# Optimization experiments

Measured on AMD Instinct MI355X. Metric: run time of the kernel, lower is better.

Reference implementation:

```python
import jax, jax.numpy as jnp
import numpy as np

# ---- static hyperparameters (mirror init_kwargs) ----
L_MAX = 3
N_MAX_L = [8, 6, 4, 2]            # radial basis size per l (precomputer.n_max_l)
N_CHANNELS = 32                   # num_element_channels
K_MAX_L = [n * N_CHANNELS for n in N_MAX_L]   # [256, 192, 128, 64]
SH_SIZES = [2 * l + 1 for l in range(L_MAX + 1)]  # [1,3,5,7]
MP_SCALING = 0.1
NU_SCALING = 0.1
NU_MAX = 2                        # max_correlation_order_per_layer
N_LAYERS = 2                      # num_message_passing_layers

# Fixed CG coupling tensors for all valid (l1, l2, L) with |l1-l2|<=L<=min(l1+l2, L_MAX).
# (Deterministic stand-ins for real Clebsch-Gordan coefficients; same sparsity/coupling
# structure and identical in fwd and fwdbwd modules.)
_rng = np.random.RandomState(0)
CG = {}
for _l1 in range(L_MAX + 1):
    for _l2 in range(L_MAX + 1):
        for _L in range(abs(_l1 - _l2), min(_l1 + _l2, L_MAX) + 1):
            CG[(_l1, _l2, _L)] = jnp.asarray(
                (_rng.randn(2 * _l1 + 1, 2 * _l2 + 1, 2 * _L + 1) * 0.2).astype(np.float32))


def split_l(x, sizes):
    out, i = [], 0
    for s in sizes:
        out.append(x[:, i:i + s])
        i += s
    return out


def embed_centers(feats, emb):
    # feats[l]: [N, 2l+1, n_l*C]; multiply channel block c by per-atom embedding emb[:, c]
    C = emb.shape[1]
    out = []
    for f in feats:
        n, m, k = f.shape
        out.append((f.reshape(n, m, k // C, C) * emb[:, None, None, :]).reshape(n, m, k))
    return out


def tensor_product(A, B):
    # per-atom CG tensor product, channel-aligned with truncation to min k
    n = A[0].shape[0]
    out = [jnp.zeros((n, 2 * L + 1, K_MAX_L[L]), A[0].dtype) for L in range(L_MAX + 1)]
    for (l1, l2, L), cg in CG.items():
        kk = min(K_MAX_L[l1], K_MAX_L[l2], K_MAX_L[L])
        t = jnp.einsum('nak,nbk,abM->nMk', A[l1][:, :, :kk], B[l2][:, :, :kk], cg)
        out[L] = out[L].at[:, :, :kk].add(t)
    return out


def cg_iterate(feats):
    # CGIterator: nu_max-1 iterated tensor products with residual accumulation
    g = feats
    for _ in range(NU_MAX - 1):
        tp = tensor_product(g, feats)
        g = [g[l] + NU_SCALING * tp[l] for l in range(L_MAX + 1)]
    return g


def invariant_mp(rb_l, sh_l, centers, emb_nbr, n_atoms):
    # spherical expansion: scatter rb x sh x neighbor-embedding over pairs -> centers
    out = []
    for l in range(L_MAX + 1):
        # [P, 2l+1, n_l, C] -> [P, 2l+1, k_l]
        msg = sh_l[l][:, :, None, None] * rb_l[l][:, None, :, None] * emb_nbr[:, None, None, :]
        msg = msg.reshape(msg.shape[0], 2 * l + 1, -1)
        out.append(MP_SCALING * jax.ops.segment_sum(msg, centers, num_segments=n_atoms))
    return out


def equivariant_mp(rb_l, sh_l, centers, neighbors, feats, n_atoms):
    # pair messages: CG-couple radially weighted SH edge features with neighbor features
    edge = [sh_l[l] * rb_l[l].sum(-1, keepdims=True) for l in range(L_MAX + 1)]  # [P, 2l+1]
    out = [jnp.zeros((n_atoms, 2 * L + 1, K_MAX_L[L]), feats[0].dtype) for L in range(L_MAX + 1)]
    for (l1, l2, L), cg in CG.items():
        kk = min(K_MAX_L[l2], K_MAX_L[L])
        w = jnp.einsum('pa,abM->pbM', edge[l1], cg)        # [P, 2l2+1, 2L+1]
        fg = feats[l2][neighbors, :, :kk]                   # gather: [P, 2l2+1, kk]
        msg = jnp.einsum('pbM,pbk->pMk', w, fg)             # [P, 2L+1, kk]
        out[L] = out[L].at[:, :, :kk].add(
            MP_SCALING * jax.ops.segment_sum(msg, centers, num_segments=n_atoms))
    return out


def setup_inputs() -> dict:
    key = jax.random.key(0)
    ks = jax.random.split(key, 8)
    N, P = 5000, 100000
    return {
        'sh': jax.random.normal(ks[0], (P, sum(SH_SIZES)), dtype=jnp.float32),
        'rb': jax.random.uniform(ks[1], (P, sum(N_MAX_L)), dtype=jnp.float32),
        'emb_table': jax.random.normal(ks[2], (4, N_CHANNELS), dtype=jnp.float32),
        'w_energy': jax.random.normal(ks[3], (K_MAX_L[0], 1), dtype=jnp.float32) * 0.05,
        'b_energy': jax.random.normal(ks[4], (1,), dtype=jnp.float32),
        'species_idx': jax.random.randint(ks[5], (N,), 0, 4, dtype=jnp.int32),
        'centers': jax.random.randint(ks[6], (P,), 0, N, dtype=jnp.int32),
        'neighbors': jax.random.randint(ks[7], (P,), 0, N, dtype=jnp.int32),
    }


def reference(sh, rb, emb_table, w_energy, b_energy, species_idx, centers, neighbors):
    n_atoms = species_idx.shape[0]
    sh_l = split_l(sh * NU_SCALING, SH_SIZES)   # nu_scaling applied to spherical harmonics
    rb_l = split_l(rb, N_MAX_L)
    center_emb = emb_table[species_idx]          # [N, C]
    emb_nbr = center_emb[neighbors]              # [P, C]
    # invariant message passing -> spherical expansion, then first CG iteration
    feats = invariant_mp(rb_l, sh_l, centers, emb_nbr, n_atoms)
    feats = cg_iterate(feats)
    # remaining equivariant message-passing layers
    for _ in range(N_LAYERS - 1):
        ef = embed_centers(feats, center_emb)
        mp = equivariant_mp(rb_l, sh_l, centers, neighbors, ef, n_atoms)
        feats = cg_iterate(mp)
    feats = embed_centers(feats, center_emb)
    energies = feats[0] @ w_energy + b_energy    # [N, 1, 1]
    return energies
```

## Files before the change

kernel.cpp:

```cpp
#include <hip/hip_runtime.h>
#include <vector>
#include <cmath>
#include <cstdint>

constexpr int KLc[4]  = {256,192,128,64};
constexpr int NMLc[4] = {8,6,4,2};
constexpr int SHBc[5] = {0,1,4,9,16};
constexpr int RBBc[5] = {0,8,14,18,20};
constexpr int FBc[5]  = {0,256,832,1472,1920};
constexpr int NCMB = 34, CGTOT = 3436, FTOT = 1920;

struct Combos { int l1[NCMB], l2[NCMB], L[NCMB], cgoff[NCMB], kk[NCMB]; };
constexpr Combos make_combos(){
  Combos c{}; int n=0, cg=0;
  for(int a=0;a<=3;a++)for(int b=0;b<=3;b++){
    int lo=a>b?a-b:b-a, hi=(a+b<3)?(a+b):3;
    for(int L=lo;L<=hi;L++){
      c.l1[n]=a; c.l2[n]=b; c.L[n]=L; c.cgoff[n]=cg;
      int mx=a>b?a:b; if(L>mx) mx=L; c.kk[n]=KLc[mx];
      cg+=(2*a+1)*(2*b+1)*(2*L+1); n++;
    }
  }
  return c;
}
constexpr Combos CB = make_combos();
static_assert(CB.cgoff[NCMB-1] + 7*7*7 == CGTOT, "cg size");

struct Grp { int cnt[4]; int list[4][12]; };
constexpr Grp make_Lg(){ Grp g{}; for(int i=0;i<NCMB;i++){ int L=CB.L[i]; g.list[L][g.cnt[L]++]=i; } return g; }
constexpr Grp LG = make_Lg();

struct Rows { int sh[64], rb[64], off[64]; };
constexpr Rows make_rows(){ Rows r{}; int i=0;
  for(int l=0;l<4;l++)for(int m=0;m<2*l+1;m++)for(int n=0;n<NMLc[l];n++){
    r.sh[i]=SHBc[l]+m; r.rb[i]=RBBc[l]+n; r.off[i]=FBc[l]+m*KLc[l]+n*32; i++; }
  for(;i<64;i++){ r.sh[i]=0; r.rb[i]=0; r.off[i]=0; }
  return r; }
constexpr Rows RWS = make_rows();

constexpr int NSL=425, NG=8, MAXS=56, MAXR=12, RPAD=149;

constexpr int iabs_(int x){ return x<0?-x:x; }
__host__ __device__ constexpr bool sl_valid(int l1,int l2,int kt){ return l2<=3-kt && iabs_(l1-l2)<=3-kt; }

__host__ __device__ constexpr int rb_base(int kt,int l1,int l2){
  int base=0;
  for(int p=0;p<4;p++)for(int q=0;q<4;q++){
    if(p==l1 && q==l2) return base;
    if(sl_valid(p,q,kt)) base += (2*p+1)*(2*q+1);
  }
  return base;
}

struct EqTab {
  int ns[NG];
  unsigned char eidx[NG][MAXS];
  unsigned char fidx[NG][MAXS];
  short         srow[NG][MAXS];
  unsigned char sph [NG][MAXS];
  int nr[NG];
  short roff[NG][MAXR];
  int total;
};
constexpr EqTab make_eqtab(){
  EqTab T{}; int gidx=0;
  for(int l2=0;l2<4;l2++)for(int kt=0;kt<4-l2;kt++)for(int b=0;b<2*l2+1;b++){
    const int rowoff = FBc[l2] + b*KLc[l2] + kt*64;
    for(int l1=0;l1<4;l1++){
      if(!sl_valid(l1,l2,kt)) continue;
      for(int a=0;a<2*l1+1;a++){
        int g = (gidx*NG)/NSL;
        int s = T.ns[g]++;
        T.eidx[g][s] = (unsigned char)(SHBc[l1]+a);
        int rbi = rb_base(kt,l1,l2) + a*(2*l2+1) + b;
        int ph, sr;
        if(kt==0){ if(l1<=2){ ph=0; sr=rbi; } else { ph=1; sr=rbi-144; } }
        else { ph=kt+1; sr=rbi; }
        T.sph[g][s]=(unsigned char)ph; T.srow[g][s]=(short)sr;
        int ri=-1;
        for(int r=0;r<T.nr[g];r++) if(T.roff[g][r]==(short)rowoff) ri=r;
        if(ri<0){ ri=T.nr[g]; T.roff[g][T.nr[g]++]=(short)rowoff; }
        T.fidx[g][s]=(unsigned char)ri;
        gidx++;
      }
    }
  }
  T.total=gidx;
  return T;
}
constexpr EqTab ET = make_eqtab();
static_assert(ET.total==NSL, "slice count");
constexpr bool chk_ns(){ for(int g=0;g<NG;g++) if(ET.ns[g]>MAXS) return false; return true; }
constexpr bool chk_nr(){ for(int g=0;g<NG;g++) if(ET.nr[g]>MAXR) return false; return true; }
static_assert(chk_ns(), "MAXS");
static_assert(chk_nr(), "MAXR");

struct CAsg { int cnt[NG]; unsigned char ci[NG][8]; };
constexpr CAsg make_casg(){
  CAsg C{}; bool used[NCMB]{}; int load[NG]{};
  for(int it=0; it<NCMB; it++){
    int best=-1, bc=-1;
    for(int i=0;i<NCMB;i++) if(!used[i]){
      int c=(2*CB.l1[i]+1)*(2*CB.l2[i]+1)*(2*CB.L[i]+1);
      if(c>bc){bc=c;best=i;}
    }
    used[best]=true;
    int g=0; for(int j=1;j<NG;j++) if(load[j]<load[g]) g=j;
    C.ci[g][C.cnt[g]++]=(unsigned char)best; load[g]+=bc;
  }
  return C;
}
constexpr CAsg CA = make_casg();
constexpr bool chk_ca(){ for(int g=0;g<NG;g++) if(CA.cnt[g]>8) return false; return true; }
static_assert(chk_ca(), "CA cap");

__host__ __device__ constexpr bool combo_in_phase(int ci,int ph){
  int l1=CB.l1[ci], l2=CB.l2[ci], L=CB.L[ci];
  if(ph==0) return l1<=2;
  if(ph==1) return l1==3;
  int kt=ph-1;
  return (l2<=3-kt) && (L<=3-kt);
}
__host__ __device__ constexpr int phase_kt(int ph){ return ph<=1?0:ph-1; }
__host__ __device__ constexpr int phase_rbadj(int ph){ return ph==1?144:0; }

namespace nprng {
struct MT {
  uint32_t mt[624]; int mti; bool has_g; double g;
  void seed(uint32_t s){ for(int i=0;i<624;i++){ mt[i]=s; s=1812433253u*(s^(s>>30))+(uint32_t)i+1u; } mti=624; has_g=false; g=0.0; }
  uint32_t u32(){
    if(mti>=624){
      for(int i=0;i<624;i++){
        uint32_t y=(mt[i]&0x80000000u)|(mt[(i+1)%624]&0x7fffffffu);
        mt[i]=mt[(i+397)%624]^(y>>1)^((y&1u)?0x9908b0dfu:0u);
      }
      mti=0;
    }
    uint32_t y=mt[mti++];
    y^=y>>11; y^=(y<<7)&0x9d2c5680u; y^=(y<<15)&0xefc60000u; y^=y>>18;
    return y;
  }
  double dbl(){ uint32_t a=u32()>>5, b=u32()>>6; return (a*67108864.0+b)/9007199254740992.0; }
  double gauss(){
    if(has_g){ has_g=false; return g; }
    double f,x1,x2,r2;
    do{ x1=2.0*dbl()-1.0; x2=2.0*dbl()-1.0; r2=x1*x1+x2*x2; }while(r2>=1.0||r2==0.0);
    f=sqrt(-2.0*log(r2)/r2);
    g=f*x1; has_g=true; return f*x2;
  }
};
}
static std::vector<float> build_cg(){
  nprng::MT r; r.seed(0);
  std::vector<float> v; v.reserve(CGTOT);
  for(int l1=0;l1<=3;l1++)for(int l2=0;l2<=3;l2++){
    int lo = l1>l2? l1-l2 : l2-l1;
    int hi = (l1+l2<3)? (l1+l2) : 3;
    for(int L=lo;L<=hi;L++){
      int n=(2*l1+1)*(2*l2+1)*(2*L+1);
      for(int i=0;i<n;i++) v.push_back((float)(r.gauss()*0.2));
    }
  }
  return v;
}

__global__ __launch_bounds__(256) void k_cemb(const float* __restrict__ emb_table,
    const int* __restrict__ species, float* __restrict__ cemb, int* __restrict__ counts, int N){
  int i = blockIdx.x*256 + threadIdx.x;
  if(i < N) counts[i] = 0;
  if(i < N*32){ int n = i>>5, c = i&31; cemb[i] = emb_table[species[n]*32 + c]; }
}

__global__ __launch_bounds__(256) void k_hist(const int* __restrict__ centers, int* counts, int P){
  int i = blockIdx.x*256 + threadIdx.x;
  if(i < P) atomicAdd(&counts[centers[i]], 1);
}

__global__ __launch_bounds__(256) void k_scan(const int* __restrict__ counts,
    int* __restrict__ offsets, int* __restrict__ cursor, int N){
  __shared__ int part[256];
  const int t = threadIdx.x;
  const int CH = (N + 255)/256;
  const int lo = t*CH;
  int hi = (t+1)*CH; if(hi > N) hi = N;
  int s = 0;
  for(int i=lo;i<hi;i++) s += counts[i];
  part[t] = s; __syncthreads();
  const int own = s;
  for(int d=1; d<256; d<<=1){
    int v = (t>=d)? part[t-d] : 0;
    __syncthreads();
    part[t] += v;
    __syncthreads();
  }
  int run = part[t] - own;
  for(int i=lo;i<hi;i++){ offsets[i]=run; cursor[i]=run; run += counts[i]; }
  if(t==255) offsets[N] = part[255];
}

__global__ __launch_bounds__(256) void k_scatter(const int* __restrict__ centers,
    int* cursor, int* __restrict__ perm, int P){
  int i = blockIdx.x*256 + threadIdx.x;
  if(i < P){ int c = centers[i]; int pos = atomicAdd(&cursor[c], 1); perm[pos] = i; }
}

__global__ __launch_bounds__(256) void k_inv(const float* __restrict__ sh, const float* __restrict__ rb,
    const float* __restrict__ cemb, const int* __restrict__ nbrs, const int* __restrict__ offsets,
    const int* __restrict__ perm, float* __restrict__ feats){
  const int a = blockIdx.x, t = threadIdx.x;
  __shared__ float sh_s[8][16], rb_s[8][20], emb_s[8][32], shrb_s[8][60];
  const int c = t & 31, rg = t >> 5;
  float acc[8];
  #pragma unroll
  for(int j=0;j<8;j++) acc[j] = 0.f;
  const int beg = offsets[a], cnt = offsets[a+1]-beg;
  for(int jb=0; jb<cnt; jb+=8){
    __syncthreads();
    for(int u=t; u<8*36; u+=256){
      int j=u/36, i=u-36*j;
      if(jb+j<cnt){
        int p=perm[beg+jb+j];
        if(i<16) sh_s[j][i]=sh[p*16+i]*0.1f;
        else     rb_s[j][i-16]=rb[p*20+i-16];
      }
    }
    for(int u=t; u<8*32; u+=256){
      int j=u>>5, i=u&31;
      if(jb+j<cnt){ int nb=nbrs[perm[beg+jb+j]]; emb_s[j][i]=cemb[(size_t)nb*32+i]; }
    }
    __syncthreads();
    for(int u=t; u<8*60; u+=256){
      int j=u/60, r=u-60*j;
      if(jb+j<cnt) shrb_s[j][r] = sh_s[j][RWS.sh[r]] * rb_s[j][RWS.rb[r]];
    }
    __syncthreads();
    const int jm = (cnt-jb<8)?(cnt-jb):8;
    for(int j=0;j<jm;j++){
      const float e = emb_s[j][c];
      #pragma unroll
      for(int q=0;q<8;q++){ int r=rg+8*q; if(r<60) acc[q]=fmaf(shrb_s[j][r], e, acc[q]); }
    }
  }
  #pragma unroll
  for(int q=0;q<8;q++){
    int r = rg + 8*q;
    if(r < 60) feats[(size_t)a*FTOT + RWS.off[r] + c] = 0.1f * acc[q];
  }
}

__device__ __forceinline__ float cg_u(const float* __restrict__ cg, int idx){
  return cg[__builtin_amdgcn_readfirstlane(idx)];
}
__global__ __launch_bounds__(256) void k_tp(float* __restrict__ feats, const float* __restrict__ cg){
  const int a = blockIdx.x, t = threadIdx.x;
  __shared__ float f_s[FTOT];
  float* fa = feats + (size_t)a*FTOT;
  for(int i=t;i<FTOT;i+=256)  f_s[i]  = fa[i];
  __syncthreads();
  #pragma unroll
  for(int L=0; L<4; L++){
    const int KLL = KLc[L], nL = 2*L+1;
    const int nel = nL*KLL;
    for(int e=t; e<nel; e+=256){
      const int M = e / KLL, k = e - M*KLL;
      float acc = 0.f;
      #pragma unroll
      for(int gi=0; gi<LG.cnt[L]; gi++){
        const int ci = LG.list[L][gi];
        const int l1 = CB.l1[ci], l2 = CB.l2[ci];
        if(k < CB.kk[ci]){
          const int n2 = 2*l2+1;
          #pragma unroll
          for(int aa=0; aa<2*l1+1; aa++){
            const float Av = f_s[FBc[l1] + aa*KLc[l1] + k];
            #pragma unroll
            for(int b=0; b<n2; b++)
              acc += cg_u(cg, CB.cgoff[ci] + (aa*n2+b)*nL + M) * (Av * f_s[FBc[l2] + b*KLc[l2] + k]);
          }
        }
      }
      fa[FBc[L] + M*KLL + k] = f_s[FBc[L] + M*KLL + k] + 0.1f*acc;
    }
  }
}

template<int G,int PH,int U>
__device__ __forceinline__ void contract_combos(const float* __restrict__ stageT,
    float* __restrict__ out_s, const float* __restrict__ cg, int lane){
  if constexpr (U < CA.cnt[G]) {
    constexpr int ci = CA.ci[G][U];
    if constexpr (combo_in_phase(ci,PH)) {
      constexpr int l1=CB.l1[ci], l2=CB.l2[ci], L=CB.L[ci];
      constexpr int n1=2*l1+1, n2=2*l2+1, nL=2*L+1;
      constexpr int kt=phase_kt(PH);
      constexpr int rbase = rb_base(kt,l1,l2) - phase_rbadj(PH);
      float oa[nL];
      #pragma unroll
      for(int M=0;M<nL;M++) oa[M]=0.f;
      #pragma unroll
      for(int aa=0;aa<n1;aa++){
        #pragma unroll
        for(int b=0;b<n2;b++){
          const float sv = stageT[lane*RPAD + rbase + aa*n2 + b];
          #pragma unroll
          for(int M=0;M<nL;M++)
            oa[M] = fmaf(cg[CB.cgoff[ci] + (aa*n2+b)*nL + M], sv, oa[M]);
        }
      }
      #pragma unroll
      for(int M=0;M<nL;M++)
        atomicAdd(&out_s[FBc[L] + M*KLc[L] + kt*64 + lane], oa[M]);
    }
    contract_combos<G,PH,U+1>(stageT,out_s,cg,lane);
  }
}

template<int G,int PH>
__device__ __forceinline__ void eq_phase(const float* acc, float* stageT, float* out_s,
    const float* __restrict__ cg, int lane){
  __syncthreads();
  #pragma unroll
  for(int s=0;s<ET.ns[G];s++){
    if(ET.sph[G][s]==PH) stageT[lane*RPAD + ET.srow[G][s]] = acc[s];
  }
  __syncthreads();
  contract_combos<G,PH,0>(stageT,out_s,cg,lane);
}

template<int G>
__device__ __forceinline__ void eq_group_main(
    const int a, const int t, const int lane,
    const float* __restrict__ sh, const float* __restrict__ rb,
    const float* __restrict__ cemb, const int* __restrict__ nbrs,
    const int* __restrict__ offsets, const int* __restrict__ perm,
    const float* __restrict__ featsA, float* __restrict__ featsB,
    const float* __restrict__ cg,
    float* stageT, float* out_s, float* edge_s, int* nb_s){
  constexpr int NS = ET.ns[G], NR = ET.nr[G];
  float acc[NS];
  #pragma unroll
  for(int s=0;s<NS;s++) acc[s]=0.f;
  for(int i=t;i<FTOT;i+=512) out_s[i]=0.f;
  const int beg = offsets[a], cnt = offsets[a+1]-beg;
  float fg_c[NR], ce_c = 0.f;
  if(cnt > 0){
    const int nb0 = nbrs[perm[beg]];
    ce_c = cemb[(size_t)nb0*32 + (lane&31)];
    const float* fp = featsA + (size_t)nb0*FTOT + lane;
    #pragma unroll
    for(int r=0;r<NR;r++) fg_c[r] = fp[ET.roff[G][r]];
  }
  for(int jb=0; jb<cnt; jb+=16){
    __syncthreads();
    if(t < 256){
      int j=t>>4, i=t&15;
      if(jb+j<cnt){
        int p = perm[beg+jb+j];
        if(i==0) nb_s[j] = nbrs[p];
        int l = (i==0)?0:(i<4)?1:(i<9)?2:3;
        float s=0.f;
        for(int n=RBBc[l]; n<RBBc[l+1]; n++) s += rb[p*20+n];
        edge_s[j*16+i] = sh[p*16+i]*0.1f*s;
      }
    }
    __syncthreads();
    const int jm = (cnt-jb<16)?(cnt-jb):16;
    for(int j=0;j<jm;j++){
      int nb_n = 0; bool have_n = true;
      if(j+1 < jm)            nb_n = nb_s[j+1];
      else if(jb+16 < cnt)    nb_n = nbrs[perm[beg+jb+16]];
      else                    have_n = false;
      float fg_n[NR], ce_n = 0.f;
      {
        const int nbl = have_n ? nb_n : 0;
        ce_n = cemb[(size_t)nbl*32 + (lane&31)];
        const float* fp = featsA + (size_t)nbl*FTOT + lane;
        #pragma unroll
        for(int r=0;r<NR;r++) fg_n[r] = fp[ET.roff[G][r]];
      }
      float ed[16];
      #pragma unroll
      for(int q=0;q<4;q++){
        float4 v = *(const float4*)(edge_s + j*16 + q*4);
        ed[q*4]=v.x; ed[q*4+1]=v.y; ed[q*4+2]=v.z; ed[q*4+3]=v.w;
      }
      float fgc[NR];
      #pragma unroll
      for(int r=0;r<NR;r++) fgc[r] = fg_c[r]*ce_c;
      #pragma unroll
      for(int s=0;s<NS;s++)
        acc[s] = fmaf(ed[ET.eidx[G][s]], fgc[ET.fidx[G][s]], acc[s]);
      #pragma unroll
      for(int r=0;r<NR;r++) fg_c[r] = fg_n[r];
      ce_c = ce_n;
    }
  }
  eq_phase<G,0>(acc,stageT,out_s,cg,lane);
  eq_phase<G,1>(acc,stageT,out_s,cg,lane);
  eq_phase<G,2>(acc,stageT,out_s,cg,lane);
  eq_phase<G,3>(acc,stageT,out_s,cg,lane);
  eq_phase<G,4>(acc,stageT,out_s,cg,lane);
  __syncthreads();
  float* ob = featsB + (size_t)a*FTOT;
  for(int i=t;i<FTOT;i+=512) ob[i] = 0.1f*out_s[i];
}

__global__ __launch_bounds__(512,4) void k_eq2(const float* __restrict__ sh, const float* __restrict__ rb,
    const float* __restrict__ cemb, const int* __restrict__ nbrs, const int* __restrict__ offsets,
    const int* __restrict__ perm, const float* __restrict__ featsA, float* __restrict__ featsB,
    const float* __restrict__ cg){
  __shared__ float stageT[64*RPAD];
  __shared__ float out_s[FTOT];
  __shared__ float edge_s[16*16];
  __shared__ int   nb_s[16];
  const int a = blockIdx.x, t = threadIdx.x, lane = t&63, g = t>>6;
  switch(g){
    case 0: eq_group_main<0>(a,t,lane,sh,rb,cemb,nbrs,offsets,perm,featsA,featsB,cg,stageT,out_s,edge_s,nb_s); break;
    case 1: eq_group_main<1>(a,t,lane,sh,rb,cemb,nbrs,offsets,perm,featsA,featsB,cg,stageT,out_s,edge_s,nb_s); break;
    case 2: eq_group_main<2>(a,t,lane,sh,rb,cemb,nbrs,offsets,perm,featsA,featsB,cg,stageT,out_s,edge_s,nb_s); break;
    case 3: eq_group_main<3>(a,t,lane,sh,rb,cemb,nbrs,offsets,perm,featsA,featsB,cg,stageT,out_s,edge_s,nb_s); break;
    case 4: eq_group_main<4>(a,t,lane,sh,rb,cemb,nbrs,offsets,perm,featsA,featsB,cg,stageT,out_s,edge_s,nb_s); break;
    case 5: eq_group_main<5>(a,t,lane,sh,rb,cemb,nbrs,offsets,perm,featsA,featsB,cg,stageT,out_s,edge_s,nb_s); break;
    case 6: eq_group_main<6>(a,t,lane,sh,rb,cemb,nbrs,offsets,perm,featsA,featsB,cg,stageT,out_s,edge_s,nb_s); break;
    default: eq_group_main<7>(a,t,lane,sh,rb,cemb,nbrs,offsets,perm,featsA,featsB,cg,stageT,out_s,edge_s,nb_s); break;
  }
}

__global__ __launch_bounds__(256) void k_energy(const float* __restrict__ feats,
    const float* __restrict__ cemb, const float* __restrict__ wE, const float* __restrict__ bE,
    float* __restrict__ out, int N){
  const int wid = threadIdx.x >> 6, lane = threadIdx.x & 63;
  const int a = blockIdx.x*4 + wid;
  if(a >= N) return;
  const float e = cemb[(size_t)a*32 + (lane & 31)];
  float s = 0.f;
  for(int k=lane; k<256; k+=64) s += feats[(size_t)a*FTOT + k] * e * wE[k];
  #pragma unroll
  for(int off=32; off; off>>=1) s += __shfl_down(s, off, 64);
  if(lane == 0) out[a] = s + bE[0];
}

extern "C" void kernel_launch(void* const* d_in, const int* in_sizes, int n_in,
                              void* d_out, int out_size, void* d_ws, size_t ws_size,
                              hipStream_t stream){
  const float* sh        = (const float*)d_in[0];
  const float* rb        = (const float*)d_in[1];
  const float* emb_table = (const float*)d_in[2];
  const float* wE        = (const float*)d_in[3];
  const float* bE        = (const float*)d_in[4];
  const int*   species   = (const int*)d_in[5];
  const int*   centers   = (const int*)d_in[6];
  const int*   nbrs      = (const int*)d_in[7];
  const int N = in_sizes[5];
  const int P = in_sizes[6];

  char* ws = (char*)d_ws; size_t off = 0;
  auto carve = [&](size_t bytes)->void*{
    void* p = ws + off; off = (off + bytes + 255) & ~(size_t)255; return p;
  };
  float* cg_d    = (float*)carve((size_t)CGTOT*4);
  float* cemb    = (float*)carve((size_t)N*32*4);
  int*   counts  = (int*)  carve((size_t)N*4);
  int*   offsets = (int*)  carve((size_t)(N+1)*4);
  int*   cursor  = (int*)  carve((size_t)N*4);
  int*   perm    = (int*)  carve((size_t)P*4);
  float* featsA  = (float*)carve((size_t)N*FTOT*4);
  float* featsB  = (float*)carve((size_t)N*FTOT*4);
  (void)ws_size; (void)n_in; (void)out_size;

  static const std::vector<float> cg_host = build_cg();
  hipMemcpyAsync(cg_d, cg_host.data(), (size_t)CGTOT*4, hipMemcpyHostToDevice, stream);

  k_cemb   <<<(N*32 + 255)/256, 256, 0, stream>>>(emb_table, species, cemb, counts, N);
  k_hist   <<<(P + 255)/256,    256, 0, stream>>>(centers, counts, P);
  k_scan   <<<1,                256, 0, stream>>>(counts, offsets, cursor, N);
  k_scatter<<<(P + 255)/256,    256, 0, stream>>>(centers, cursor, perm, P);
  k_inv    <<<N,                256, 0, stream>>>(sh, rb, cemb, nbrs, offsets, perm, featsA);
  k_tp     <<<N,                256, 0, stream>>>(featsA, cg_d);
  k_eq2    <<<N,                512, 0, stream>>>(sh, rb, cemb, nbrs, offsets, perm, featsA, featsB, cg_d);
  k_tp     <<<N,                256, 0, stream>>>(featsB, cg_d);
  k_energy <<<(N + 3)/4,        256, 0, stream>>>(featsB, cemb, wE, bE, (float*)d_out, N);
}
```

Before: 936.2 us.

## Fold center embedding into tensor-product output and deepen neighbor gather prefetch

The per-atom center-embedding multiply moves into the k_tp epilogue, so the message-passing kernel no longer reloads and multiplies the neighbor embedding per edge, and the energy kernel drops its embedding multiply. The neighbor loop in k_eq2 now caches up to 128 neighbor indices in shared memory and keeps a three-deep register ring of prefetched neighbor features, unrolled across 12-edge chunks. Slice tables are sorted so that entries sharing the same edge and feature index sit next to each other. CG loads no longer use readfirstlane. In exchange, register pressure rises with the 3x NR prefetch buffers, and the edge chunk shrinks from 16 to 12.

```diff
diff --git a/kernel.cpp b/kernel.cpp
--- a/kernel.cpp
+++ b/kernel.cpp
@@ -86,6 +86,20 @@
     }
   }
   T.total=gidx;
+  for(int g=0; g<NG; g++){
+    for(int i=1;i<T.ns[g];i++){
+      for(int j=i; j>0; j--){
+        int kj = T.eidx[g][j]*64 + T.fidx[g][j];
+        int kp = T.eidx[g][j-1]*64 + T.fidx[g][j-1];
+        if(kj < kp){
+          unsigned char te=T.eidx[g][j]; T.eidx[g][j]=T.eidx[g][j-1]; T.eidx[g][j-1]=te;
+          unsigned char tf=T.fidx[g][j]; T.fidx[g][j]=T.fidx[g][j-1]; T.fidx[g][j-1]=tf;
+          short ts=T.srow[g][j]; T.srow[g][j]=T.srow[g][j-1]; T.srow[g][j-1]=ts;
+          unsigned char tp=T.sph[g][j]; T.sph[g][j]=T.sph[g][j-1]; T.sph[g][j-1]=tp;
+        } else break;
+      }
+    }
+  }
   return T;
 }
 constexpr EqTab ET = make_eqtab();
@@ -248,13 +262,13 @@
   }
 }
 
-__device__ __forceinline__ float cg_u(const float* __restrict__ cg, int idx){
-  return cg[__builtin_amdgcn_readfirstlane(idx)];
-}
-__global__ __launch_bounds__(256) void k_tp(float* __restrict__ feats, const float* __restrict__ cg){
+__global__ __launch_bounds__(256) void k_tp(float* __restrict__ feats, const float* __restrict__ cg,
+    const float* __restrict__ cemb){
   const int a = blockIdx.x, t = threadIdx.x;
   __shared__ float f_s[FTOT];
+  __shared__ float cemb_s[32];
   float* fa = feats + (size_t)a*FTOT;
+  if(t < 32) cemb_s[t] = cemb[(size_t)a*32 + t];
   for(int i=t;i<FTOT;i+=256)  f_s[i]  = fa[i];
   __syncthreads();
   #pragma unroll
@@ -275,11 +289,11 @@
             const float Av = f_s[FBc[l1] + aa*KLc[l1] + k];
             #pragma unroll
             for(int b=0; b<n2; b++)
-              acc += cg_u(cg, CB.cgoff[ci] + (aa*n2+b)*nL + M) * (Av * f_s[FBc[l2] + b*KLc[l2] + k]);
+              acc += cg[CB.cgoff[ci] + (aa*n2+b)*nL + M] * (Av * f_s[FBc[l2] + b*KLc[l2] + k]);
           }
         }
       }
-      fa[FBc[L] + M*KLL + k] = f_s[FBc[L] + M*KLL + k] + 0.1f*acc;
+      fa[FBc[L] + M*KLL + k] = (f_s[FBc[L] + M*KLL + k] + 0.1f*acc) * cemb_s[k & 31];
     }
   }
 }
@@ -327,72 +341,77 @@
   contract_combos<G,PH,0>(stageT,out_s,cg,lane);
 }
 
+template<int G,int U>
+__device__ __forceinline__ void pair_steps(
+    float* __restrict__ acc, float (*__restrict__ fg)[ET.nr[G]],
+    const float* __restrict__ featsA, const int* __restrict__ nbrs,
+    const int* __restrict__ perm, const int* __restrict__ nb_s,
+    const float* __restrict__ edge_s,
+    const int jb, const int beg, const int cnt, const int lane){
+  if constexpr (U < 12){
+    constexpr int NS = ET.ns[G], NR = ET.nr[G];
+    constexpr int s = U % 3;
+    float ed[16];
+    #pragma unroll
+    for(int q=0;q<4;q++){
+      float4 v = *(const float4*)(edge_s + U*16 + q*4);
+      ed[q*4]=v.x; ed[q*4+1]=v.y; ed[q*4+2]=v.z; ed[q*4+3]=v.w;
+    }
+    #pragma unroll
+    for(int q=0;q<NS;q++)
+      acc[q] = fmaf(ed[ET.eidx[G][q]], fg[s][ET.fidx[G][q]], acc[q]);
+    int jn = jb+U+3; if(jn > cnt-1) jn = cnt-1;
+    const int nb = (jn < 128) ? nb_s[jn] : nbrs[perm[beg+jn]];
+    const float* fp = featsA + (size_t)nb*FTOT + lane;
+    #pragma unroll
+    for(int r=0;r<NR;r++) fg[s][r] = fp[ET.roff[G][r]];
+    pair_steps<G,U+1>(acc,fg,featsA,nbrs,perm,nb_s,edge_s,jb,beg,cnt,lane);
+  }
+}
+
 template<int G>
 __device__ __forceinline__ void eq_group_main(
     const int a, const int t, const int lane,
     const float* __restrict__ sh, const float* __restrict__ rb,
-    const float* __restrict__ cemb, const int* __restrict__ nbrs,
-    const int* __restrict__ offsets, const int* __restrict__ perm,
+    const int* __restrict__ nbrs, const int* __restrict__ offsets,
+    const int* __restrict__ perm,
     const float* __restrict__ featsA, float* __restrict__ featsB,
     const float* __restrict__ cg,
     float* stageT, float* out_s, float* edge_s, int* nb_s){
   constexpr int NS = ET.ns[G], NR = ET.nr[G];
   float acc[NS];
   #pragma unroll
-  for(int s=0;s<NS;s++) acc[s]=0.f;
+  for(int q=0;q<NS;q++) acc[q]=0.f;
   for(int i=t;i<FTOT;i+=512) out_s[i]=0.f;
   const int beg = offsets[a], cnt = offsets[a+1]-beg;
-  float fg_c[NR], ce_c = 0.f;
+  const int nbcap = cnt<128?cnt:128;
+  for(int i=t;i<nbcap;i+=512) nb_s[i] = nbrs[perm[beg+i]];
+  __syncthreads();
   if(cnt > 0){
-    const int nb0 = nbrs[perm[beg]];
-    ce_c = cemb[(size_t)nb0*32 + (lane&31)];
-    const float* fp = featsA + (size_t)nb0*FTOT + lane;
+    float fg[3][NR];
     #pragma unroll
-    for(int r=0;r<NR;r++) fg_c[r] = fp[ET.roff[G][r]];
-  }
-  for(int jb=0; jb<cnt; jb+=16){
-    __syncthreads();
-    if(t < 256){
-      int j=t>>4, i=t&15;
-      if(jb+j<cnt){
-        int p = perm[beg+jb+j];
-        if(i==0) nb_s[j] = nbrs[p];
-        int l = (i==0)?0:(i<4)?1:(i<9)?2:3;
-        float s=0.f;
-        for(int n=RBBc[l]; n<RBBc[l+1]; n++) s += rb[p*20+n];
-        edge_s[j*16+i] = sh[p*16+i]*0.1f*s;
-      }
-    }
-    __syncthreads();
-    const int jm = (cnt-jb<16)?(cnt-jb):16;
-    for(int j=0;j<jm;j++){
-      int nb_n = 0; bool have_n = true;
-      if(j+1 < jm)            nb_n = nb_s[j+1];
-      else if(jb+16 < cnt)    nb_n = nbrs[perm[beg+jb+16]];
-      else                    have_n = false;
-      float fg_n[NR], ce_n = 0.f;
-      {
-        const int nbl = have_n ? nb_n : 0;
-        ce_n = cemb[(size_t)nbl*32 + (lane&31)];
-        const float* fp = featsA + (size_t)nbl*FTOT + lane;
-        #pragma unroll
-        for(int r=0;r<NR;r++) fg_n[r] = fp[ET.roff[G][r]];
-      }
-      float ed[16];
+    for(int s=0;s<3;s++){
+      const int jj = (s<cnt)? s : cnt-1;
+      const float* fp = featsA + (size_t)nb_s[jj]*FTOT + lane;
       #pragma unroll
-      for(int q=0;q<4;q++){
-        float4 v = *(const float4*)(edge_s + j*16 + q*4);
-        ed[q*4]=v.x; ed[q*4+1]=v.y; ed[q*4+2]=v.z; ed[q*4+3]=v.w;
-      }
-      float fgc[NR];
-      #pragma unroll
-      for(int r=0;r<NR;r++) fgc[r] = fg_c[r]*ce_c;
-      #pragma unroll
-      for(int s=0;s<NS;s++)
-        acc[s] = fmaf(ed[ET.eidx[G][s]], fgc[ET.fidx[G][s]], acc[s]);
-      #pragma unroll
-      for(int r=0;r<NR;r++) fg_c[r] = fg_n[r];
-      ce_c = ce_n;
+      for(int r=0;r<NR;r++) fg[s][r] = fp[ET.roff[G][r]];
+    }
+    for(int jb=0; jb<cnt; jb+=12){
+      __syncthreads();
+      if(t < 192){
+        const int j=t>>4, i=t&15, jj=jb+j;
+        float ev = 0.f;
+        if(jj < cnt){
+          const int p = perm[beg+jj];
+          const int l = (i==0)?0:(i<4)?1:(i<9)?2:3;
+          float ssum = 0.f;
+          for(int n=RBBc[l]; n<RBBc[l+1]; n++) ssum += rb[p*20+n];
+          ev = sh[p*16+i]*0.1f*ssum;
+        }
+        edge_s[j*16+i] = ev;
+      }
+      __syncthreads();
+      pair_steps<G,0>(acc,fg,featsA,nbrs,perm,nb_s,edge_s,jb,beg,cnt,lane);
     }
   }
   eq_phase<G,0>(acc,stageT,out_s,cg,lane);
@@ -406,35 +425,34 @@
 }
 
 __global__ __launch_bounds__(512,4) void k_eq2(const float* __restrict__ sh, const float* __restrict__ rb,
-    const float* __restrict__ cemb, const int* __restrict__ nbrs, const int* __restrict__ offsets,
+    const int* __restrict__ nbrs, const int* __restrict__ offsets,
     const int* __restrict__ perm, const float* __restrict__ featsA, float* __restrict__ featsB,
     const float* __restrict__ cg){
   __shared__ float stageT[64*RPAD];
   __shared__ float out_s[FTOT];
-  __shared__ float edge_s[16*16];
-  __shared__ int   nb_s[16];
+  __shared__ float edge_s[12*16];
+  __shared__ int   nb_s[128];
   const int a = blockIdx.x, t = threadIdx.x, lane = t&63, g = t>>6;
   switch(g){
-    case 0: eq_group_main<0>(a,t,lane,sh,rb,cemb,nbrs,offsets,perm,featsA,featsB,cg,stageT,out_s,edge_s,nb_s); break;
-    case 1: eq_group_main<1>(a,t,lane,sh,rb,cemb,nbrs,offsets,perm,featsA,featsB,cg,stageT,out_s,edge_s,nb_s); break;
-    case 2: eq_group_main<2>(a,t,lane,sh,rb,cemb,nbrs,offsets,perm,featsA,featsB,cg,stageT,out_s,edge_s,nb_s); break;
-    case 3: eq_group_main<3>(a,t,lane,sh,rb,cemb,nbrs,offsets,perm,featsA,featsB,cg,stageT,out_s,edge_s,nb_s); break;
-    case 4: eq_group_main<4>(a,t,lane,sh,rb,cemb,nbrs,offsets,perm,featsA,featsB,cg,stageT,out_s,edge_s,nb_s); break;
-    case 5: eq_group_main<5>(a,t,lane,sh,rb,cemb,nbrs,offsets,perm,featsA,featsB,cg,stageT,out_s,edge_s,nb_s); break;
-    case 6: eq_group_main<6>(a,t,lane,sh,rb,cemb,nbrs,offsets,perm,featsA,featsB,cg,stageT,out_s,edge_s,nb_s); break;
-    default: eq_group_main<7>(a,t,lane,sh,rb,cemb,nbrs,offsets,perm,featsA,featsB,cg,stageT,out_s,edge_s,nb_s); break;
+    case 0: eq_group_main<0>(a,t,lane,sh,rb,nbrs,offsets,perm,featsA,featsB,cg,stageT,out_s,edge_s,nb_s); break;
+    case 1: eq_group_main<1>(a,t,lane,sh,rb,nbrs,offsets,perm,featsA,featsB,cg,stageT,out_s,edge_s,nb_s); break;
+    case 2: eq_group_main<2>(a,t,lane,sh,rb,nbrs,offsets,perm,featsA,featsB,cg,stageT,out_s,edge_s,nb_s); break;
+    case 3: eq_group_main<3>(a,t,lane,sh,rb,nbrs,offsets,perm,featsA,featsB,cg,stageT,out_s,edge_s,nb_s); break;
+    case 4: eq_group_main<4>(a,t,lane,sh,rb,nbrs,offsets,perm,featsA,featsB,cg,stageT,out_s,edge_s,nb_s); break;
+    case 5: eq_group_main<5>(a,t,lane,sh,rb,nbrs,offsets,perm,featsA,featsB,cg,stageT,out_s,edge_s,nb_s); break;
+    case 6: eq_group_main<6>(a,t,lane,sh,rb,nbrs,offsets,perm,featsA,featsB,cg,stageT,out_s,edge_s,nb_s); break;
+    default: eq_group_main<7>(a,t,lane,sh,rb,nbrs,offsets,perm,featsA,featsB,cg,stageT,out_s,edge_s,nb_s); break;
   }
 }
 
 __global__ __launch_bounds__(256) void k_energy(const float* __restrict__ feats,
-    const float* __restrict__ cemb, const float* __restrict__ wE, const float* __restrict__ bE,
+    const float* __restrict__ wE, const float* __restrict__ bE,
     float* __restrict__ out, int N){
   const int wid = threadIdx.x >> 6, lane = threadIdx.x & 63;
   const int a = blockIdx.x*4 + wid;
   if(a >= N) return;
-  const float e = cemb[(size_t)a*32 + (lane & 31)];
   float s = 0.f;
-  for(int k=lane; k<256; k+=64) s += feats[(size_t)a*FTOT + k] * e * wE[k];
+  for(int k=lane; k<256; k+=64) s += feats[(size_t)a*FTOT + k] * wE[k];
   #pragma unroll
   for(int off=32; off; off>>=1) s += __shfl_down(s, off, 64);
   if(lane == 0) out[a] = s + bE[0];
@@ -476,8 +494,8 @@
   k_scan   <<<1,                256, 0, stream>>>(counts, offsets, cursor, N);
   k_scatter<<<(P + 255)/256,    256, 0, stream>>>(centers, cursor, perm, P);
   k_inv    <<<N,                256, 0, stream>>>(sh, rb, cemb, nbrs, offsets, perm, featsA);
-  k_tp     <<<N,                256, 0, stream>>>(featsA, cg_d);
-  k_eq2    <<<N,                512, 0, stream>>>(sh, rb, cemb, nbrs, offsets, perm, featsA, featsB, cg_d);
-  k_tp     <<<N,                256, 0, stream>>>(featsB, cg_d);
-  k_energy <<<(N + 3)/4,        256, 0, stream>>>(featsB, cemb, wE, bE, (float*)d_out, N);
-}
+  k_tp     <<<N,                256, 0, stream>>>(featsA, cg_d, cemb);
+  k_eq2    <<<N,                512, 0, stream>>>(sh, rb, nbrs, offsets, perm, featsA, featsB, cg_d);
+  k_tp     <<<N,                256, 0, stream>>>(featsB, cg_d, cemb);
+  k_energy <<<(N + 3)/4,        256, 0, stream>>>(featsB, wE, bE, (float*)d_out, N);
+}
```

Result: slower. 2.948 ms (+214.9%).
